# Kernel tuning notes

Hardware: AMD Instinct MI355X
Metric: run time of the kernel (lower is better)

## Reference

```python
import jax, jax.numpy as jnp
import numpy as np

B, L, H, E = 4, 2048, 16, 64
S, D = L, E

def setup_inputs() -> dict:
    key = jax.random.key(0)
    kq, kk, kv = jax.random.split(key, 3)
    queries = jax.random.normal(kq, (B, L, H, E), dtype=jnp.float32)
    keys = jax.random.normal(kk, (B, S, H, E), dtype=jnp.float32)
    values = jax.random.normal(kv, (B, S, H, D), dtype=jnp.float32)
    return {"queries": queries, "keys": keys, "values": values}

def reference(queries, keys, values):
    # FullAttention with mask_flag=True, attn_mask=None -> causal mask; dropout p=0 (eval).
    b, l, h, e = queries.shape
    scale = 1.0 / jnp.sqrt(jnp.asarray(e, queries.dtype))
    # scores: [B,H,L,S]
    scores = jnp.einsum('blhe,bshe->bhls', queries, keys)
    causal = jnp.triu(jnp.ones((l, l), dtype=bool), k=1)  # True above diagonal -> masked
    scores = jnp.where(causal[None, None, :, :], -jnp.inf, scores)
    A = jax.nn.softmax(scale * scores, axis=-1)
    V = jnp.einsum('bhls,bshd->blhd', A, values)
    return V
```

## Files before the change

### kernel.cpp

```cpp
#include <hip/hip_runtime.h>
#include <math.h>

#define BB 4
#define LL 2048
#define HH 16
#define EE 64
#define HE (HH*EE)

constexpr int QBLK  = 128;
constexpr int KVBLK = 64;
constexpr int NW    = 8;
constexpr int NQT   = LL / QBLK;
constexpr int LDK   = 72;
constexpr float SCL2E = 0.18033688011112042f;
constexpr float DEFER_THR = 8.0f;

typedef short short8 __attribute__((ext_vector_type(8)));
typedef float f32x4  __attribute__((ext_vector_type(4)));

#define MFMA(a, b, c) __builtin_amdgcn_mfma_f32_16x16x32_bf16((a), (b), (c), 0, 0, 0)

static __device__ __forceinline__ unsigned short f2bf(float f) {
    unsigned u = __float_as_uint(f);
    return (unsigned short)((u + 0x7FFFu + ((u >> 16) & 1u)) >> 16);
}

__global__ __launch_bounds__(512, 4)
void attn_mfma(const float* __restrict__ Q, const float* __restrict__ K,
               const float* __restrict__ V, float* __restrict__ O)
{
    __shared__ short Ks[KVBLK * LDK];
    __shared__ short Vt[EE * LDK];
    __shared__ short Pl[NW * 16 * LDK];

    const int bid = blockIdx.x;
    const int qt  = (NQT - 1) - (bid >> 6);
    const int bh  = bid & 63;
    const int b   = bh >> 4, h = bh & 15;
    const size_t base = (size_t)b * LL * HE + (size_t)h * EE;

    const int tid  = threadIdx.x;
    const int wave = tid >> 6, lane = tid & 63;
    const int g    = lane >> 4, c = lane & 15;

    const int q0 = qt * QBLK + wave * 16;

    short8 qf[2];
    {
        const float* qp = Q + base + (size_t)(q0 + c) * HE + 8 * g;
        #pragma unroll
        for (int ec = 0; ec < 2; ++ec) {
            float4 f0 = *(const float4*)(qp + ec * 32);
            float4 f1 = *(const float4*)(qp + ec * 32 + 4);
            float fv[8] = {f0.x, f0.y, f0.z, f0.w, f1.x, f1.y, f1.z, f1.w};
            #pragma unroll
            for (int i = 0; i < 8; ++i)
                qf[ec][i] = (short)f2bf(fv[i] * SCL2E);
        }
    }

    f32x4 o[4];
    #pragma unroll
    for (int db = 0; db < 4; ++db)
        #pragma unroll
        for (int j = 0; j < 4; ++j) o[db][j] = 0.0f;
    float m_r[4] = {-INFINITY, -INFINITY, -INFINITY, -INFINITY};
    float l_r[4] = {0.f, 0.f, 0.f, 0.f};

    const int ntile = 2 * qt + 2;
    const int srow = tid >> 3;
    const int scc  = (tid & 7) * 8;

    for (int t = 0; t < ntile; ++t) {
        const int j0 = t * KVBLK;

        __syncthreads();
        {
            const float* kp = K + base + (size_t)(j0 + srow) * HE + scc;
            float4 a0 = *(const float4*)(kp);
            float4 a1 = *(const float4*)(kp + 4);
            float fv[8] = {a0.x, a0.y, a0.z, a0.w, a1.x, a1.y, a1.z, a1.w};
            short8 hv;
            #pragma unroll
            for (int i = 0; i < 8; ++i) hv[i] = (short)f2bf(fv[i]);
            *(short8*)(&Ks[srow * LDK + scc]) = hv;

            const float* vp = V + base + (size_t)(j0 + srow) * HE + scc;
            float4 b0 = *(const float4*)(vp);
            float4 b1 = *(const float4*)(vp + 4);
            float gv[8] = {b0.x, b0.y, b0.z, b0.w, b1.x, b1.y, b1.z, b1.w};
            #pragma unroll
            for (int i = 0; i < 8; ++i) {
                const int d = scc + i;
                const int col = srow ^ (((d >> 3) & 7) << 3);
                Vt[d * LDK + col] = (short)f2bf(gv[i]);
            }
        }
        __syncthreads();

        if (j0 <= q0 + 15) {
            const bool diag = (j0 + KVBLK - 1) > q0;

            f32x4 s[4];
            __builtin_amdgcn_s_setprio(1);
            #pragma unroll
            for (int kb = 0; kb < 4; ++kb) {
                f32x4 acc; acc[0]=0.f; acc[1]=0.f; acc[2]=0.f; acc[3]=0.f;
                const int roff = (kb * 16 + c) * LDK + 8 * g;
                short8 k0 = *(const short8*)(&Ks[roff]);
                short8 k1 = *(const short8*)(&Ks[roff + 32]);
                acc = MFMA(qf[0], k0, acc);
                acc = MFMA(qf[1], k1, acc);
                s[kb] = acc;
            }
            __builtin_amdgcn_s_setprio(0);

            float tm[4];
            #pragma unroll
            for (int r = 0; r < 4; ++r) {
                if (diag) {
                    const int qrow = q0 + 4 * g + r;
                    #pragma unroll
                    for (int kb = 0; kb < 4; ++kb)
                        if (j0 + kb * 16 + c > qrow) s[kb][r] = -INFINITY;
                }
                tm[r] = fmaxf(fmaxf(s[0][r], s[1][r]), fmaxf(s[2][r], s[3][r]));
                #pragma unroll
                for (int xm = 1; xm <= 8; xm <<= 1)
                    tm[r] = fmaxf(tm[r], __shfl_xor(tm[r], xm));
            }

            #pragma unroll
            for (int r = 0; r < 4; ++r) {
                const float nm = fmaxf(m_r[r], tm[r]);
                if (nm - m_r[r] > DEFER_THR) {
                    const float corr = __builtin_amdgcn_exp2f(m_r[r] - nm);
                    l_r[r] *= corr;
                    #pragma unroll
                    for (int db = 0; db < 4; ++db) o[db][r] *= corr;
                    m_r[r] = nm;
                }
                #pragma unroll
                for (int kb = 0; kb < 4; ++kb) {
                    const float p = __builtin_amdgcn_exp2f(s[kb][r] - m_r[r]);
                    l_r[r] += p;
                    Pl[(wave * 16 + 4 * g + r) * LDK + kb * 16 + c] = (short)f2bf(p);
                }
            }

            #pragma unroll
            for (int kc = 0; kc < 2; ++kc) {
                short8 pa = *(const short8*)(&Pl[(wave * 16 + c) * LDK + kc * 32 + 8 * g]);
                __builtin_amdgcn_s_setprio(1);
                #pragma unroll
                for (int db = 0; db < 4; ++db) {
                    const int d  = db * 16 + c;
                    const int k0 = (kc * 32 + 8 * g) ^ (((d >> 3) & 7) << 3);
                    short8 vb = *(const short8*)(&Vt[d * LDK + k0]);
                    o[db] = MFMA(pa, vb, o[db]);
                }
                __builtin_amdgcn_s_setprio(0);
            }
        }
    }

    #pragma unroll
    for (int r = 0; r < 4; ++r) {
        float ls = l_r[r];
        #pragma unroll
        for (int xm = 1; xm <= 8; xm <<= 1) ls += __shfl_xor(ls, xm);
        const float inv = 1.0f / ls;
        float* op = O + base + (size_t)(q0 + 4 * g + r) * HE + c;
        #pragma unroll
        for (int db = 0; db < 4; ++db)
            op[db * 16] = o[db][r] * inv;
    }
}

extern "C" void kernel_launch(void* const* d_in, const int* in_sizes, int n_in,
                              void* d_out, int out_size, void* d_ws, size_t ws_size,
                              hipStream_t stream) {
    const float* Q = (const float*)d_in[0];
    const float* K = (const float*)d_in[1];
    const float* V = (const float*)d_in[2];
    float* Out = (float*)d_out;

    dim3 grid(BB * HH * NQT);
    dim3 block(512);
    hipLaunchKernelGGL(attn_mfma, grid, block, 0, stream, Q, K, V, Out);
}
```

Baseline: 225.4 us.

## Pre-convert K/V to swizzled bf16 tiles and load via global_load_lds

Adds a prepass kernel that converts K and V to bf16 once, stores them in per-tile swizzled layout (V transposed) in the workspace. The attention kernel then loads each tile directly into LDS with global_load_lds instead of repeatedly loading fp32 and converting per query block. This removes redundant conversion and halves KV read bytes across the many query tiles, at the cost of an extra kernel launch and workspace traffic. Falls back to the old kernel if workspace is too small.

```diff
diff --git a/kernel.cpp b/kernel.cpp
--- a/kernel.cpp
+++ b/kernel.cpp
@@ -11,6 +11,7 @@
 constexpr int KVBLK = 64;
 constexpr int NW    = 8;
 constexpr int NQT   = LL / QBLK;
+constexpr int NT    = LL / KVBLK;
 constexpr int LDK   = 72;
 constexpr float SCL2E = 0.18033688011112042f;
 constexpr float DEFER_THR = 8.0f;
@@ -20,9 +21,192 @@
 
 #define MFMA(a, b, c) __builtin_amdgcn_mfma_f32_16x16x32_bf16((a), (b), (c), 0, 0, 0)
 
+#define GLD_LDS16(gp, lp)                                                     \
+    __builtin_amdgcn_global_load_lds(                                         \
+        (const __attribute__((address_space(1))) void*)(gp),                  \
+        (__attribute__((address_space(3))) void*)(lp), 16, 0, 0)
+
 static __device__ __forceinline__ unsigned short f2bf(float f) {
     unsigned u = __float_as_uint(f);
     return (unsigned short)((u + 0x7FFFu + ((u >> 16) & 1u)) >> 16);
+}
+
+__global__ __launch_bounds__(512, 2)
+void prepass_cvt(const float* __restrict__ K, const float* __restrict__ V,
+                 short* __restrict__ Kw, short* __restrict__ Vw)
+{
+    __shared__ short Vs[KVBLK][74];
+    const int bid = blockIdx.x;
+    const int bh  = bid >> 5, t = bid & 31;
+    const int b   = bh >> 4, h = bh & 15;
+    const int j0  = t * KVBLK;
+    const int tid = threadIdx.x;
+    const int row = tid >> 3;
+    const int ch8 = (tid & 7) * 8;
+    const size_t gbase = (size_t)b * LL * HE + (size_t)h * EE;
+    const size_t obase = (size_t)bid * (64 * 64);
+
+    {
+        const float* kp = K + gbase + (size_t)(j0 + row) * HE + ch8;
+        float4 a0 = *(const float4*)kp, a1 = *(const float4*)(kp + 4);
+        float fv[8] = {a0.x,a0.y,a0.z,a0.w,a1.x,a1.y,a1.z,a1.w};
+        short8 hv;
+        #pragma unroll
+        for (int i = 0; i < 8; ++i) hv[i] = (short)f2bf(fv[i]);
+        *(short8*)(Kw + obase + row * 64 + (ch8 ^ ((row & 7) * 8))) = hv;
+    }
+    {
+        const float* vp = V + gbase + (size_t)(j0 + row) * HE + ch8;
+        float4 b0 = *(const float4*)vp, b1 = *(const float4*)(vp + 4);
+        float gv[8] = {b0.x,b0.y,b0.z,b0.w,b1.x,b1.y,b1.z,b1.w};
+        short8 vv;
+        #pragma unroll
+        for (int i = 0; i < 8; ++i) vv[i] = (short)f2bf(gv[i]);
+        *(short8*)(&Vs[row][ch8]) = vv;
+    }
+    __syncthreads();
+    {
+        short8 ov;
+        #pragma unroll
+        for (int i = 0; i < 8; ++i) ov[i] = Vs[ch8 + i][row];
+        *(short8*)(Vw + obase + row * 64 + (ch8 ^ ((row & 7) * 8))) = ov;
+    }
+}
+
+__global__ __launch_bounds__(512, 4)
+void attn_fast(const float* __restrict__ Q, const short* __restrict__ Kw,
+               const short* __restrict__ Vw, float* __restrict__ O)
+{
+    __shared__ alignas(16) short Ks[KVBLK * 64];
+    __shared__ alignas(16) short Vt[EE * 64];
+    __shared__ short Pl[NW * 16 * LDK];
+
+    const int bid = blockIdx.x;
+    const int qt  = (NQT - 1) - (bid >> 6);
+    const int bh  = bid & 63;
+    const int b   = bh >> 4, h = bh & 15;
+    const size_t base = (size_t)b * LL * HE + (size_t)h * EE;
+
+    const int tid  = threadIdx.x;
+    const int wave = tid >> 6, lane = tid & 63;
+    const int g    = lane >> 4, c = lane & 15;
+    const int swz  = (c & 7) * 8;
+
+    const int q0 = qt * QBLK + wave * 16;
+    const size_t kvbase = (size_t)bh * (NT * 64 * 64);
+
+    short8 qf[2];
+    {
+        const float* qp = Q + base + (size_t)(q0 + c) * HE + 8 * g;
+        #pragma unroll
+        for (int ec = 0; ec < 2; ++ec) {
+            float4 f0 = *(const float4*)(qp + ec * 32);
+            float4 f1 = *(const float4*)(qp + ec * 32 + 4);
+            float fv[8] = {f0.x, f0.y, f0.z, f0.w, f1.x, f1.y, f1.z, f1.w};
+            #pragma unroll
+            for (int i = 0; i < 8; ++i)
+                qf[ec][i] = (short)f2bf(fv[i] * SCL2E);
+        }
+    }
+
+    f32x4 o[4];
+    #pragma unroll
+    for (int db = 0; db < 4; ++db)
+        #pragma unroll
+        for (int j = 0; j < 4; ++j) o[db][j] = 0.0f;
+    float m_r[4] = {-INFINITY, -INFINITY, -INFINITY, -INFINITY};
+    float l_r[4] = {0.f, 0.f, 0.f, 0.f};
+
+    const int ntile = 2 * qt + 2;
+
+    for (int t = 0; t < ntile; ++t) {
+        const int j0 = t * KVBLK;
+
+        __syncthreads();
+        {
+            const size_t goff = kvbase + (size_t)t * 4096
+                              + (size_t)(wave * 64 + lane) * 8;
+            GLD_LDS16(Kw + goff, Ks + wave * 512);
+            GLD_LDS16(Vw + goff, Vt + wave * 512);
+        }
+        __syncthreads();
+
+        if (j0 <= q0 + 15) {
+            const bool diag = (j0 + KVBLK - 1) > q0;
+
+            f32x4 s[4];
+            __builtin_amdgcn_s_setprio(1);
+            #pragma unroll
+            for (int kb = 0; kb < 4; ++kb) {
+                f32x4 acc; acc[0]=0.f; acc[1]=0.f; acc[2]=0.f; acc[3]=0.f;
+                const int roff = (kb * 16 + c) * 64;
+                short8 k0 = *(const short8*)(&Ks[roff + ((8 * g) ^ swz)]);
+                short8 k1 = *(const short8*)(&Ks[roff + ((32 + 8 * g) ^ swz)]);
+                acc = MFMA(qf[0], k0, acc);
+                acc = MFMA(qf[1], k1, acc);
+                s[kb] = acc;
+            }
+            __builtin_amdgcn_s_setprio(0);
+
+            float tm[4];
+            #pragma unroll
+            for (int r = 0; r < 4; ++r) {
+                if (diag) {
+                    const int qrow = q0 + 4 * g + r;
+                    #pragma unroll
+                    for (int kb = 0; kb < 4; ++kb)
+                        if (j0 + kb * 16 + c > qrow) s[kb][r] = -INFINITY;
+                }
+                tm[r] = fmaxf(fmaxf(s[0][r], s[1][r]), fmaxf(s[2][r], s[3][r]));
+                #pragma unroll
+                for (int xm = 1; xm <= 8; xm <<= 1)
+                    tm[r] = fmaxf(tm[r], __shfl_xor(tm[r], xm));
+            }
+
+            #pragma unroll
+            for (int r = 0; r < 4; ++r) {
+                const float nm = fmaxf(m_r[r], tm[r]);
+                if (nm - m_r[r] > DEFER_THR) {
+                    const float corr = __builtin_amdgcn_exp2f(m_r[r] - nm);
+                    l_r[r] *= corr;
+                    #pragma unroll
+                    for (int db = 0; db < 4; ++db) o[db][r] *= corr;
+                    m_r[r] = nm;
+                }
+                #pragma unroll
+                for (int kb = 0; kb < 4; ++kb) {
+                    const float p = __builtin_amdgcn_exp2f(s[kb][r] - m_r[r]);
+                    l_r[r] += p;
+                    Pl[(wave * 16 + 4 * g + r) * LDK + kb * 16 + c] = (short)f2bf(p);
+                }
+            }
+
+            #pragma unroll
+            for (int kc = 0; kc < 2; ++kc) {
+                short8 pa = *(const short8*)(&Pl[(wave * 16 + c) * LDK + kc * 32 + 8 * g]);
+                __builtin_amdgcn_s_setprio(1);
+                #pragma unroll
+                for (int db = 0; db < 4; ++db) {
+                    const int voff = (db * 16 + c) * 64 + ((kc * 32 + 8 * g) ^ swz);
+                    short8 vb = *(const short8*)(&Vt[voff]);
+                    o[db] = MFMA(pa, vb, o[db]);
+                }
+                __builtin_amdgcn_s_setprio(0);
+            }
+        }
+    }
+
+    #pragma unroll
+    for (int r = 0; r < 4; ++r) {
+        float ls = l_r[r];
+        #pragma unroll
+        for (int xm = 1; xm <= 8; xm <<= 1) ls += __shfl_xor(ls, xm);
+        const float inv = 1.0f / ls;
+        float* op = O + base + (size_t)(q0 + 4 * g + r) * HE + c;
+        #pragma unroll
+        for (int db = 0; db < 4; ++db)
+            op[db * 16] = o[db][r] * inv;
+    }
 }
 
 __global__ __launch_bounds__(512, 4)
@@ -185,7 +369,15 @@
     const float* V = (const float*)d_in[2];
     float* Out = (float*)d_out;
 
-    dim3 grid(BB * HH * NQT);
-    dim3 block(512);
-    hipLaunchKernelGGL(attn_mfma, grid, block, 0, stream, Q, K, V, Out);
-}
+    const size_t kv_shorts = (size_t)64 * NT * 64 * 64;
+    const size_t need = 2 * kv_shorts * sizeof(short);
+
+    if (ws_size >= need) {
+        short* Kw = (short*)d_ws;
+        short* Vw = Kw + kv_shorts;
+        hipLaunchKernelGGL(prepass_cvt, dim3(64 * NT), dim3(512), 0, stream, K, V, Kw, Vw);
+        hipLaunchKernelGGL(attn_fast, dim3(BB * HH * NQT), dim3(512), 0, stream, Q, Kw, Vw, Out);
+    } else {
+        hipLaunchKernelGGL(attn_mfma, dim3(BB * HH * NQT), dim3(512), 0, stream, Q, K, V, Out);
+    }
+}
```

Result: faster. 213.0 us (-5.5%).
